# Kernel optimization log

Hardware: AMD Instinct MI355X
Metric: run time of the kernel (lower is better)

## Reference

```python
import jax, jax.numpy as jnp
import numpy as np

B, LQ, LKV, D, H = 4, 1024, 2048, 1024, 16
HD = D // H
EPS = 1e-5
NEG = -1e9


def _layernorm(x, w, b):
    mu = jnp.mean(x, axis=-1, keepdims=True)
    var = jnp.mean(jnp.square(x - mu), axis=-1, keepdims=True)
    return (x - mu) * jax.lax.rsqrt(var + EPS) * w + b


def setup_inputs() -> dict:
    key = jax.random.key(0)
    ks = jax.random.split(key, 10)
    q = jax.random.normal(ks[0], (B, LQ, D), dtype=jnp.float32)
    kv = jax.random.normal(ks[1], (B, LKV, D), dtype=jnp.float32)
    # ragged kv lengths; mask True == padding
    lengths = jax.random.randint(ks[2], (B,), LKV // 4, LKV + 1)
    mask = jnp.arange(LKV)[None, :] >= lengths[:, None]  # [B, LKV] bool
    s = 1.0 / np.sqrt(D)
    params = dict(
        norm_q_w=jnp.ones((D,), jnp.float32),
        norm_q_b=jnp.zeros((D,), jnp.float32),
        norm_kv_w=jnp.ones((D,), jnp.float32),
        norm_kv_b=jnp.zeros((D,), jnp.float32),
        Wq=jax.random.normal(ks[3], (D, D), jnp.float32) * s,
        bq=jnp.zeros((D,), jnp.float32),
        Wkv=jax.random.normal(ks[4], (2 * D, D), jnp.float32) * s,
        bkv=jnp.zeros((2 * D,), jnp.float32),
        Wo=jax.random.normal(ks[5], (D, D), jnp.float32) * s,
        bo=jnp.zeros((D,), jnp.float32),
    )
    return dict(q=q, kv=kv, mask=mask, **params)


def reference(q, kv, mask, norm_q_w, norm_q_b, norm_kv_w, norm_kv_b, Wq, bq, Wkv, bkv, Wo, bo):
    q_res = q
    qn = _layernorm(q, norm_q_w, norm_q_b)
    kvn = _layernorm(kv, norm_kv_w, norm_kv_b)
    # projections
    qh = (qn @ Wq.T + bq).reshape(B, LQ, H, HD)
    kvp = (kvn @ Wkv.T + bkv).reshape(B, LKV, 2, H, HD)
    k, v = kvp[:, :, 0], kvp[:, :, 1]  # [B, LKV, H, HD]
    # masked cross attention (math-equivalent to varlen flash attn over unpadded kv)
    scale = 1.0 / np.sqrt(HD)
    scores = jnp.einsum('bqhd,bkhd->bhqk', qh, k) * scale
    scores = jnp.where(mask[:, None, None, :], NEG, scores)
    attn = jax.nn.softmax(scores, axis=-1)
    out = jnp.einsum('bhqk,bkhd->bqhd', attn, v).reshape(B, LQ, D)
    # out proj + residual (dropout is identity in eval)
    return q_res + (out @ Wo.T + bo)


if __name__ == '__main__':
    inp = setup_inputs()
    y = reference(**inp)
    print(y.shape, y.dtype)
```

## Files before the change

kernel.cpp:

```cpp
#include <hip/hip_runtime.h>

#define DEV __device__ __forceinline__

typedef unsigned short u16;
typedef float  floatx4 __attribute__((ext_vector_type(4)));
typedef unsigned int uintx4 __attribute__((ext_vector_type(4)));
typedef __bf16 bf16x8 __attribute__((ext_vector_type(8)));

constexpr int cB = 4, cLQ = 1024, cLKV = 2048, cD = 1024, cH = 16, cHD = 64;

DEV u16 f2bf(float f) {
  unsigned u = __builtin_bit_cast(unsigned, f);
  u += 0x7fffu + ((u >> 16) & 1u);
  return (u16)(u >> 16);
}

DEV float bf2f(u16 u) {
  return __builtin_bit_cast(float, (unsigned)u << 16);
}

DEV bf16x8 ld_frag(const u16* p) {
  uintx4 u = *(const uintx4*)p;
  return __builtin_bit_cast(bf16x8, u);
}

DEV floatx4 mfma16(bf16x8 a, bf16x8 b, floatx4 c) {
  return __builtin_amdgcn_mfma_f32_16x16x32_bf16(a, b, c, 0, 0, 0);
}

__global__ __launch_bounds__(256) void ln_all_kernel(
    const float* __restrict__ q, const float* __restrict__ kv,
    const float* __restrict__ nqw, const float* __restrict__ nqb,
    const float* __restrict__ nkw, const float* __restrict__ nkb,
    u16* __restrict__ qn, u16* __restrict__ kvn) {
  int row = blockIdx.x, tid = threadIdx.x;
  const float* x; const float* w; const float* b; u16* dst;
  if (row < cB * cLQ) {
    x = q + (size_t)row * cD; w = nqw; b = nqb; dst = qn + (size_t)row * cD;
  } else {
    int r2 = row - cB * cLQ;
    x = kv + (size_t)r2 * cD; w = nkw; b = nkb; dst = kvn + (size_t)r2 * cD;
  }
  float4 v = ((const float4*)x)[tid];
  __shared__ float sbuf[8];
  float s = v.x + v.y + v.z + v.w;
  #pragma unroll
  for (int m = 1; m < 64; m <<= 1) s += __shfl_xor(s, m, 64);
  if ((tid & 63) == 0) sbuf[tid >> 6] = s;
  __syncthreads();
  float mean = (sbuf[0] + sbuf[1] + sbuf[2] + sbuf[3]) * (1.f / cD);
  float dx = v.x - mean, dy = v.y - mean, dz = v.z - mean, dw = v.w - mean;
  float ss = dx * dx + dy * dy + dz * dz + dw * dw;
  #pragma unroll
  for (int m = 1; m < 64; m <<= 1) ss += __shfl_xor(ss, m, 64);
  if ((tid & 63) == 0) sbuf[4 + (tid >> 6)] = ss;
  __syncthreads();
  float var = (sbuf[4] + sbuf[5] + sbuf[6] + sbuf[7]) * (1.f / cD);
  float rs = rsqrtf(var + 1e-5f);
  float4 wv = ((const float4*)w)[tid];
  float4 bv = ((const float4*)b)[tid];
  ushort4 o;
  o.x = f2bf(dx * rs * wv.x + bv.x);
  o.y = f2bf(dy * rs * wv.y + bv.y);
  o.z = f2bf(dz * rs * wv.z + bv.z);
  o.w = f2bf(dw * rs * wv.w + bv.w);
  ((ushort4*)dst)[tid] = o;
}

__global__ __launch_bounds__(256) void cast_lens_kernel(
    const float* __restrict__ Wq, const float* __restrict__ Wkv,
    const float* __restrict__ Wo, u16* __restrict__ wqb,
    u16* __restrict__ wkvb, u16* __restrict__ wob,
    const void* __restrict__ mask, int* __restrict__ lens) {
  int tid = threadIdx.x;
  if (blockIdx.x == 4096) {
    __shared__ int smode;
    __shared__ int cnt[cB];
    if (tid == 0) smode = 0;
    if (tid < cB) cnt[tid] = 0;
    __syncthreads();
    const unsigned* mi = (const unsigned*)mask;
    int bad = 0;
    for (int i = tid; i < cB * cLKV / 4; i += 256)
      if (mi[i] > 1u) bad = 1;
    if (bad) smode = 1;
    __syncthreads();
    if (smode == 0) {
      for (int b = 0; b < cB; b++) {
        int c = 0;
        for (int i = tid; i < cLKV; i += 256) c += (mi[(size_t)b * cLKV + i] == 0u);
        atomicAdd(&cnt[b], c);
      }
    } else {
      const unsigned char* m8 = (const unsigned char*)mask;
      for (int b = 0; b < cB; b++) {
        int c = 0;
        for (int i = tid; i < cLKV; i += 256) c += (m8[(size_t)b * cLKV + i] == 0);
        atomicAdd(&cnt[b], c);
      }
    }
    __syncthreads();
    if (tid < cB) lens[tid] = cnt[tid];
    return;
  }
  int gi = blockIdx.x * 256 + tid;
  const float* src; u16* dst; int off;
  if (gi < 262144)      { src = Wq;  dst = wqb;  off = gi; }
  else if (gi < 786432) { src = Wkv; dst = wkvb; off = gi - 262144; }
  else                  { src = Wo;  dst = wob;  off = gi - 786432; }
  float4 v = ((const float4*)src)[off];
  ushort4 o;
  o.x = f2bf(v.x); o.y = f2bf(v.y); o.z = f2bf(v.z); o.w = f2bf(v.w);
  ((ushort4*)dst)[off] = o;
}

struct TileCtx {
  int m16, quad, wr, wc;
};

DEV void gemm_mainloop(const u16* __restrict__ A, const u16* __restrict__ Bm,
                       int row0, int col0, int K, u16* As, u16* Bs,
                       const TileCtx& t, floatx4 (&acc)[4][4]) {
  int tid = threadIdx.x;
  int wave = tid >> 6, lane = tid & 63;
  int srow = wave * 16 + (lane >> 2);
  int sseg = (lane & 3) * 8;
  const u16* ga = A + (size_t)(row0 + srow) * K + sseg;
  const u16* gb = Bm + (size_t)(col0 + srow) * K + sseg;
  const size_t rstep = (size_t)64 * K;
  u16* wA = As + srow * 32 + sseg;
  u16* wB = Bs + srow * 32 + sseg;

  uintx4 a0 = *(const uintx4*)ga;
  uintx4 a1 = *(const uintx4*)(ga + rstep);
  uintx4 b0 = *(const uintx4*)gb;
  uintx4 b1 = *(const uintx4*)(gb + rstep);

  for (int k0 = 0; k0 < K; k0 += 32) {
    __syncthreads();
    *(uintx4*)wA = a0;
    *(uintx4*)(wA + 64 * 32) = a1;
    *(uintx4*)wB = b0;
    *(uintx4*)(wB + 64 * 32) = b1;
    if (k0 + 32 < K) {
      a0 = *(const uintx4*)(ga + k0 + 32);
      a1 = *(const uintx4*)(ga + rstep + k0 + 32);
      b0 = *(const uintx4*)(gb + k0 + 32);
      b1 = *(const uintx4*)(gb + rstep + k0 + 32);
    }
    __syncthreads();
    bf16x8 af[4], bfr[4];
    #pragma unroll
    for (int i = 0; i < 4; i++)
      af[i] = ld_frag(&As[(t.wr * 64 + i * 16 + t.m16) * 32 + t.quad * 8]);
    #pragma unroll
    for (int j = 0; j < 4; j++)
      bfr[j] = ld_frag(&Bs[(t.wc * 64 + j * 16 + t.m16) * 32 + t.quad * 8]);
    #pragma unroll
    for (int i = 0; i < 4; i++)
      #pragma unroll
      for (int j = 0; j < 4; j++)
        acc[i][j] = mfma16(af[i], bfr[j], acc[i][j]);
  }
}

__global__ __launch_bounds__(256) void proj_fused(
    const u16* __restrict__ qn, const u16* __restrict__ wqb,
    const float* __restrict__ bq, u16* __restrict__ qhb,
    const u16* __restrict__ kvn, const u16* __restrict__ wkvb,
    const float* __restrict__ bkv, u16* __restrict__ khb,
    u16* __restrict__ vthb) {
  __shared__ __align__(16) u16 As[128 * 32];
  __shared__ __align__(16) u16 Bs[128 * 32];
  int bid = blockIdx.x;
  int lane = threadIdx.x & 63;
  TileCtx t;
  t.m16 = lane & 15; t.quad = lane >> 4;
  int wave = threadIdx.x >> 6;
  t.wr = wave >> 1; t.wc = wave & 1;

  bool isQ = bid < 256;
  int row0, col0;
  const u16* A; const u16* Bm; const float* bias;
  if (isQ) {
    row0 = (bid >> 3) * 128; col0 = (bid & 7) * 128;
    A = qn; Bm = wqb; bias = bq;
  } else {
    int b2 = bid - 256;
    row0 = (b2 >> 4) * 128; col0 = (b2 & 15) * 128;
    A = kvn; Bm = wkvb; bias = bkv;
  }

  floatx4 z = {0.f, 0.f, 0.f, 0.f};
  floatx4 acc[4][4];
  #pragma unroll
  for (int i = 0; i < 4; i++)
    #pragma unroll
    for (int j = 0; j < 4; j++) acc[i][j] = z;

  gemm_mainloop(A, Bm, row0, col0, cD, As, Bs, t, acc);

  #pragma unroll
  for (int j = 0; j < 4; j++) {
    int col = col0 + t.wc * 64 + j * 16 + t.m16;
    float bs = bias[col];
    if (isQ) {
      #pragma unroll
      for (int i = 0; i < 4; i++) {
        int crow = row0 + t.wr * 64 + i * 16 + t.quad * 4;
        #pragma unroll
        for (int r = 0; r < 4; r++)
          qhb[(size_t)(crow + r) * cD + col] = f2bf((acc[i][j][r] + bs) * 0.125f);
      }
    } else {
      bool isK = col < cD;
      int c2 = isK ? col : col - cD;
      int hh = c2 >> 6, dd = c2 & 63;
      #pragma unroll
      for (int i = 0; i < 4; i++) {
        int crow = row0 + t.wr * 64 + i * 16 + t.quad * 4;
        int bb = crow >> 11, kvp = crow & (cLKV - 1);
        if (isK) {
          u16* dst = khb + ((size_t)(bb * cH + hh) * cLKV + kvp) * 64 + dd;
          #pragma unroll
          for (int r = 0; r < 4; r++) dst[(size_t)r * 64] = f2bf(acc[i][j][r] + bs);
        } else {
          u16* dst = vthb + ((size_t)(bb * cH + hh) * 64 + dd) * cLKV + kvp;
          ushort4 o;
          o.x = f2bf(acc[i][j][0] + bs);
          o.y = f2bf(acc[i][j][1] + bs);
          o.z = f2bf(acc[i][j][2] + bs);
          o.w = f2bf(acc[i][j][3] + bs);
          *(ushort4*)dst = o;
        }
      }
    }
  }
}

__global__ __launch_bounds__(256) void gemm_o(
    const u16* __restrict__ A, const u16* __restrict__ Bm,
    const float* __restrict__ bias, const float* __restrict__ res,
    float* __restrict__ Cout, int N, int K) {
  __shared__ __align__(16) u16 As[128 * 32];
  __shared__ __align__(16) u16 Bs[128 * 32];
  int lane = threadIdx.x & 63;
  TileCtx t;
  t.m16 = lane & 15; t.quad = lane >> 4;
  int wave = threadIdx.x >> 6;
  t.wr = wave >> 1; t.wc = wave & 1;
  int row0 = blockIdx.y * 128, col0 = blockIdx.x * 128;

  floatx4 z = {0.f, 0.f, 0.f, 0.f};
  floatx4 acc[4][4];
  #pragma unroll
  for (int i = 0; i < 4; i++)
    #pragma unroll
    for (int j = 0; j < 4; j++) acc[i][j] = z;

  gemm_mainloop(A, Bm, row0, col0, K, As, Bs, t, acc);

  #pragma unroll
  for (int j = 0; j < 4; j++) {
    int col = col0 + t.wc * 64 + j * 16 + t.m16;
    float bs = bias[col];
    #pragma unroll
    for (int i = 0; i < 4; i++) {
      int crow = row0 + t.wr * 64 + i * 16 + t.quad * 4;
      #pragma unroll
      for (int r = 0; r < 4; r++) {
        size_t idx = (size_t)(crow + r) * N + col;
        Cout[idx] = acc[i][j][r] + bs + res[idx];
      }
    }
  }
}

constexpr int KS = 72;

template<bool MASK>
DEV void attn_compute(int k0g, int len, const u16* __restrict__ Kt,
                      const u16* __restrict__ Vt, u16* __restrict__ psw,
                      bf16x8 aq0, bf16x8 aq1, int m16, int quad,
                      float (&lsum)[4], floatx4 (&accO)[4]) {
  floatx4 z = {0.f, 0.f, 0.f, 0.f};
  floatx4 s[4];
  #pragma unroll
  for (int t = 0; t < 4; t++) {
    bf16x8 bk0 = ld_frag(&Kt[(t * 16 + m16) * KS + quad * 8]);
    bf16x8 bk1 = ld_frag(&Kt[(t * 16 + m16) * KS + 32 + quad * 8]);
    floatx4 tt = z;
    tt = mfma16(aq0, bk0, tt);
    tt = mfma16(aq1, bk1, tt);
    s[t] = tt;
  }
  #pragma unroll
  for (int r = 0; r < 4; r++) {
    float e0, e1, e2, e3;
    if (MASK) {
      int key = k0g + m16;
      e0 = (key < len) ? __expf(s[0][r]) : 0.f;
      e1 = (key + 16 < len) ? __expf(s[1][r]) : 0.f;
      e2 = (key + 32 < len) ? __expf(s[2][r]) : 0.f;
      e3 = (key + 48 < len) ? __expf(s[3][r]) : 0.f;
    } else {
      e0 = __expf(s[0][r]);
      e1 = __expf(s[1][r]);
      e2 = __expf(s[2][r]);
      e3 = __expf(s[3][r]);
    }
    lsum[r] += (e0 + e1) + (e2 + e3);
    int prow = (quad * 4 + r) * KS + m16;
    psw[prow] = f2bf(e0);
    psw[prow + 16] = f2bf(e1);
    psw[prow + 32] = f2bf(e2);
    psw[prow + 48] = f2bf(e3);
  }
  bf16x8 ap0 = ld_frag(&psw[m16 * KS + quad * 8]);
  bf16x8 ap1 = ld_frag(&psw[m16 * KS + 32 + quad * 8]);
  #pragma unroll
  for (int db = 0; db < 4; db++) {
    bf16x8 bv0 = ld_frag(&Vt[(db * 16 + m16) * KS + quad * 8]);
    bf16x8 bv1 = ld_frag(&Vt[(db * 16 + m16) * KS + 32 + quad * 8]);
    accO[db] = mfma16(ap0, bv0, accO[db]);
    accO[db] = mfma16(ap1, bv1, accO[db]);
  }
}

__global__ __launch_bounds__(256) void attn_kernel(
    const u16* __restrict__ qh, const u16* __restrict__ kh,
    const u16* __restrict__ vth, const int* __restrict__ lens,
    u16* __restrict__ op, float* __restrict__ ls) {
  int gid = blockIdx.x;
  int b = gid & (cB - 1);
  int s = (gid >> 2) & 1;
  int h = (gid >> 3) & (cH - 1);
  int qt = gid >> 7;
  int len = lens[b];
  int koff = s << 10;
  int lim = min(len, koff + 1024);
  int nch = (lim > koff) ? ((lim - koff + 63) >> 6) : 0;

  int wave = threadIdx.x >> 6, lane = threadIdx.x & 63;
  int m16 = lane & 15, quad = lane >> 4;

  __shared__ __align__(16) u16 Kt[64 * KS];
  __shared__ __align__(16) u16 Vt[64 * KS];
  __shared__ __align__(16) u16 Ps[4][16 * KS];
  u16* psw = &Ps[wave][0];

  int qrow = qt * 64 + wave * 16 + m16;
  const u16* qp = qh + ((size_t)(b * cLQ + qrow) * cH + h) * cHD;
  bf16x8 aq0 = ld_frag(qp + quad * 8);
  bf16x8 aq1 = ld_frag(qp + 32 + quad * 8);

  const u16* kbase = kh + (size_t)(b * cH + h) * cLKV * cHD;
  const u16* vbase = vth + (size_t)(b * cH + h) * cHD * cLKV;

  int srow = threadIdx.x >> 3;
  int sseg = threadIdx.x & 7;
  const u16* kg0 = kbase + (size_t)srow * cHD + sseg * 8;
  const u16* vg0 = vbase + (size_t)srow * cLKV + sseg * 8;

  float lsum[4] = {0.f, 0.f, 0.f, 0.f};
  floatx4 z = {0.f, 0.f, 0.f, 0.f};
  floatx4 accO[4] = {z, z, z, z};

  uintx4 ka  = *(const uintx4*)(kg0 + (size_t)koff * cHD);
  uintx4 kb2 = *(const uintx4*)(kg0 + (size_t)(koff + 32) * cHD);
  uintx4 va  = *(const uintx4*)(vg0 + koff);
  uintx4 vb  = *(const uintx4*)(vg0 + (size_t)32 * cLKV + koff);

  for (int c = 0; c < nch; c++) {
    int k0g = koff + c * 64;
    __syncthreads();
    *(uintx4*)&Kt[srow * KS + sseg * 8] = ka;
    *(uintx4*)&Kt[(srow + 32) * KS + sseg * 8] = kb2;
    *(uintx4*)&Vt[srow * KS + sseg * 8] = va;
    *(uintx4*)&Vt[(srow + 32) * KS + sseg * 8] = vb;
    if (c + 1 < nch) {
      int kn = k0g + 64;
      ka  = *(const uintx4*)(kg0 + (size_t)kn * cHD);
      kb2 = *(const uintx4*)(kg0 + (size_t)(kn + 32) * cHD);
      va  = *(const uintx4*)(vg0 + kn);
      vb  = *(const uintx4*)(vg0 + (size_t)32 * cLKV + kn);
    }
    __syncthreads();
    if (k0g + 64 <= len)
      attn_compute<false>(k0g, len, Kt, Vt, psw, aq0, aq1, m16, quad, lsum, accO);
    else
      attn_compute<true>(k0g, len, Kt, Vt, psw, aq0, aq1, m16, quad, lsum, accO);
  }

  #pragma unroll
  for (int r = 0; r < 4; r++) {
    float t = lsum[r];
    #pragma unroll
    for (int m = 1; m < 16; m <<= 1) t += __shfl_xor(t, m, 64);
    lsum[r] = t;
  }

  #pragma unroll
  for (int r = 0; r < 4; r++) {
    int qg = qt * 64 + wave * 16 + quad * 4 + r;
    size_t rowidx = (size_t)(b * cLQ + qg);
    if (m16 == 0)
      ls[(size_t)s * cB * cLQ * cH + rowidx * cH + h] = lsum[r];
    size_t base = ((size_t)s * cB * cLQ + rowidx) * cD + h * 64;
    #pragma unroll
    for (int db = 0; db < 4; db++)
      op[base + db * 16 + m16] = f2bf(accO[db][r]);
  }
}

__global__ __launch_bounds__(256) void combine_kernel(
    const u16* __restrict__ op, const float* __restrict__ ls,
    u16* __restrict__ aob) {
  int row = blockIdx.x;
  int t = threadIdx.x;
  int h = t >> 4;
  float l = ls[(size_t)row * cH + h] + ls[(size_t)cB * cLQ * cH + (size_t)row * cH + h];
  float inv = 1.0f / l;
  size_t i0 = (size_t)row * cD + t * 4;
  ushort4 a = *(const ushort4*)(op + i0);
  ushort4 b2 = *(const ushort4*)(op + (size_t)cB * cLQ * cD + i0);
  ushort4 o;
  o.x = f2bf((bf2f(a.x) + bf2f(b2.x)) * inv);
  o.y = f2bf((bf2f(a.y) + bf2f(b2.y)) * inv);
  o.z = f2bf((bf2f(a.z) + bf2f(b2.z)) * inv);
  o.w = f2bf((bf2f(a.w) + bf2f(b2.w)) * inv);
  *(ushort4*)(aob + i0) = o;
}

extern "C" void kernel_launch(void* const* d_in, const int* in_sizes, int n_in,
                              void* d_out, int out_size, void* d_ws, size_t ws_size,
                              hipStream_t stream) {
  const float* q    = (const float*)d_in[0];
  const float* kv   = (const float*)d_in[1];
  const void*  mask = d_in[2];
  const float* nqw  = (const float*)d_in[3];
  const float* nqb  = (const float*)d_in[4];
  const float* nkw  = (const float*)d_in[5];
  const float* nkb  = (const float*)d_in[6];
  const float* Wq   = (const float*)d_in[7];
  const float* bq   = (const float*)d_in[8];
  const float* Wkv  = (const float*)d_in[9];
  const float* bkv  = (const float*)d_in[10];
  const float* Wo   = (const float*)d_in[11];
  const float* bo   = (const float*)d_in[12];
  float* out = (float*)d_out;

  char* w = (char*)d_ws;
  int* lens = (int*)w;       w += 256;
  u16* qn   = (u16*)w;       w += (size_t)cB * cLQ * cD * 2;
  u16* kvn  = (u16*)w;       w += (size_t)cB * cLKV * cD * 2;
  u16* wqb  = (u16*)w;       w += (size_t)cD * cD * 2;
  u16* wkvb = (u16*)w;       w += (size_t)2 * cD * cD * 2;
  u16* wob  = (u16*)w;       w += (size_t)cD * cD * 2;
  u16* qhb  = (u16*)w;       w += (size_t)cB * cLQ * cD * 2;
  u16* khb  = (u16*)w;       w += (size_t)cB * cH * cLKV * cHD * 2;
  u16* vthb = (u16*)w;       w += (size_t)cB * cH * cHD * cLKV * 2;
  u16* aob  = (u16*)w;       w += (size_t)cB * cLQ * cD * 2;
  u16* opart = (u16*)w;      w += (size_t)2 * cB * cLQ * cD * 2;
  float* lspart = (float*)w;

  ln_all_kernel<<<cB * (cLQ + cLKV), 256, 0, stream>>>(
      q, kv, nqw, nqb, nkw, nkb, qn, kvn);
  cast_lens_kernel<<<4097, 256, 0, stream>>>(
      Wq, Wkv, Wo, wqb, wkvb, wob, mask, lens);
  proj_fused<<<1280, 256, 0, stream>>>(
      qn, wqb, bq, qhb, kvn, wkvb, bkv, khb, vthb);
  attn_kernel<<<2048, 256, 0, stream>>>(
      qhb, khb, vthb, lens, opart, lspart);
  combine_kernel<<<cB * cLQ, 256, 0, stream>>>(opart, lspart, aob);
  gemm_o<<<dim3(cD / 128, cB * cLQ / 128), 256, 0, stream>>>(
      aob, wob, bo, q, out, cD, cD);
}
```

Measured before the change: 315.6 us.

## Merge prep kernels, double-buffer GEMM LDS, drop attention KV split and combine

```diff
diff --git a/kernel.cpp b/kernel.cpp
--- a/kernel.cpp
+++ b/kernel.cpp
@@ -15,8 +15,8 @@
   return (u16)(u >> 16);
 }
 
-DEV float bf2f(u16 u) {
-  return __builtin_bit_cast(float, (unsigned)u << 16);
+DEV u16 f2bf_t(float f) {
+  return (u16)(__builtin_bit_cast(unsigned, f) >> 16);
 }
 
 DEV bf16x8 ld_frag(const u16* p) {
@@ -28,52 +28,59 @@
   return __builtin_amdgcn_mfma_f32_16x16x32_bf16(a, b, c, 0, 0, 0);
 }
 
-__global__ __launch_bounds__(256) void ln_all_kernel(
+__global__ __launch_bounds__(256) void prep_kernel(
     const float* __restrict__ q, const float* __restrict__ kv,
     const float* __restrict__ nqw, const float* __restrict__ nqb,
     const float* __restrict__ nkw, const float* __restrict__ nkb,
-    u16* __restrict__ qn, u16* __restrict__ kvn) {
-  int row = blockIdx.x, tid = threadIdx.x;
-  const float* x; const float* w; const float* b; u16* dst;
-  if (row < cB * cLQ) {
-    x = q + (size_t)row * cD; w = nqw; b = nqb; dst = qn + (size_t)row * cD;
-  } else {
-    int r2 = row - cB * cLQ;
-    x = kv + (size_t)r2 * cD; w = nkw; b = nkb; dst = kvn + (size_t)r2 * cD;
-  }
-  float4 v = ((const float4*)x)[tid];
-  __shared__ float sbuf[8];
-  float s = v.x + v.y + v.z + v.w;
-  #pragma unroll
-  for (int m = 1; m < 64; m <<= 1) s += __shfl_xor(s, m, 64);
-  if ((tid & 63) == 0) sbuf[tid >> 6] = s;
-  __syncthreads();
-  float mean = (sbuf[0] + sbuf[1] + sbuf[2] + sbuf[3]) * (1.f / cD);
-  float dx = v.x - mean, dy = v.y - mean, dz = v.z - mean, dw = v.w - mean;
-  float ss = dx * dx + dy * dy + dz * dz + dw * dw;
-  #pragma unroll
-  for (int m = 1; m < 64; m <<= 1) ss += __shfl_xor(ss, m, 64);
-  if ((tid & 63) == 0) sbuf[4 + (tid >> 6)] = ss;
-  __syncthreads();
-  float var = (sbuf[4] + sbuf[5] + sbuf[6] + sbuf[7]) * (1.f / cD);
-  float rs = rsqrtf(var + 1e-5f);
-  float4 wv = ((const float4*)w)[tid];
-  float4 bv = ((const float4*)b)[tid];
-  ushort4 o;
-  o.x = f2bf(dx * rs * wv.x + bv.x);
-  o.y = f2bf(dy * rs * wv.y + bv.y);
-  o.z = f2bf(dz * rs * wv.z + bv.z);
-  o.w = f2bf(dw * rs * wv.w + bv.w);
-  ((ushort4*)dst)[tid] = o;
-}
-
-__global__ __launch_bounds__(256) void cast_lens_kernel(
+    u16* __restrict__ qn, u16* __restrict__ kvn,
     const float* __restrict__ Wq, const float* __restrict__ Wkv,
     const float* __restrict__ Wo, u16* __restrict__ wqb,
     u16* __restrict__ wkvb, u16* __restrict__ wob,
     const void* __restrict__ mask, int* __restrict__ lens) {
-  int tid = threadIdx.x;
-  if (blockIdx.x == 4096) {
+  int bid = blockIdx.x, tid = threadIdx.x;
+  if (bid < cB * (cLQ + cLKV)) {
+    const float* x; const float* w; const float* b; u16* dst;
+    if (bid < cB * cLQ) {
+      x = q + (size_t)bid * cD; w = nqw; b = nqb; dst = qn + (size_t)bid * cD;
+    } else {
+      int r2 = bid - cB * cLQ;
+      x = kv + (size_t)r2 * cD; w = nkw; b = nkb; dst = kvn + (size_t)r2 * cD;
+    }
+    float4 v = ((const float4*)x)[tid];
+    __shared__ float sbuf[8];
+    float s = v.x + v.y + v.z + v.w;
+    #pragma unroll
+    for (int m = 1; m < 64; m <<= 1) s += __shfl_xor(s, m, 64);
+    if ((tid & 63) == 0) sbuf[tid >> 6] = s;
+    __syncthreads();
+    float mean = (sbuf[0] + sbuf[1] + sbuf[2] + sbuf[3]) * (1.f / cD);
+    float dx = v.x - mean, dy = v.y - mean, dz = v.z - mean, dw = v.w - mean;
+    float ss = dx * dx + dy * dy + dz * dz + dw * dw;
+    #pragma unroll
+    for (int m = 1; m < 64; m <<= 1) ss += __shfl_xor(ss, m, 64);
+    if ((tid & 63) == 0) sbuf[4 + (tid >> 6)] = ss;
+    __syncthreads();
+    float var = (sbuf[4] + sbuf[5] + sbuf[6] + sbuf[7]) * (1.f / cD);
+    float rs = rsqrtf(var + 1e-5f);
+    float4 wv = ((const float4*)w)[tid];
+    float4 bv = ((const float4*)b)[tid];
+    ushort4 o;
+    o.x = f2bf(dx * rs * wv.x + bv.x);
+    o.y = f2bf(dy * rs * wv.y + bv.y);
+    o.z = f2bf(dz * rs * wv.z + bv.z);
+    o.w = f2bf(dw * rs * wv.w + bv.w);
+    ((ushort4*)dst)[tid] = o;
+  } else if (bid < cB * (cLQ + cLKV) + 4096) {
+    int gi = (bid - cB * (cLQ + cLKV)) * 256 + tid;
+    const float* src; u16* dst; int off;
+    if (gi < 262144)      { src = Wq;  dst = wqb;  off = gi; }
+    else if (gi < 786432) { src = Wkv; dst = wkvb; off = gi - 262144; }
+    else                  { src = Wo;  dst = wob;  off = gi - 786432; }
+    float4 v = ((const float4*)src)[off];
+    ushort4 o;
+    o.x = f2bf(v.x); o.y = f2bf(v.y); o.z = f2bf(v.z); o.w = f2bf(v.w);
+    ((ushort4*)dst)[off] = o;
+  } else {
     __shared__ int smode;
     __shared__ int cnt[cB];
     if (tid == 0) smode = 0;
@@ -101,17 +108,7 @@
     }
     __syncthreads();
     if (tid < cB) lens[tid] = cnt[tid];
-    return;
-  }
-  int gi = blockIdx.x * 256 + tid;
-  const float* src; u16* dst; int off;
-  if (gi < 262144)      { src = Wq;  dst = wqb;  off = gi; }
-  else if (gi < 786432) { src = Wkv; dst = wkvb; off = gi - 262144; }
-  else                  { src = Wo;  dst = wob;  off = gi - 786432; }
-  float4 v = ((const float4*)src)[off];
-  ushort4 o;
-  o.x = f2bf(v.x); o.y = f2bf(v.y); o.z = f2bf(v.z); o.w = f2bf(v.w);
-  ((ushort4*)dst)[off] = o;
+  }
 }
 
 struct TileCtx {
@@ -128,39 +125,53 @@
   const u16* ga = A + (size_t)(row0 + srow) * K + sseg;
   const u16* gb = Bm + (size_t)(col0 + srow) * K + sseg;
   const size_t rstep = (size_t)64 * K;
-  u16* wA = As + srow * 32 + sseg;
-  u16* wB = Bs + srow * 32 + sseg;
+  int woff = srow * 32 + sseg;
 
   uintx4 a0 = *(const uintx4*)ga;
   uintx4 a1 = *(const uintx4*)(ga + rstep);
   uintx4 b0 = *(const uintx4*)gb;
   uintx4 b1 = *(const uintx4*)(gb + rstep);
+  *(uintx4*)(As + woff) = a0;
+  *(uintx4*)(As + woff + 2048) = a1;
+  *(uintx4*)(Bs + woff) = b0;
+  *(uintx4*)(Bs + woff + 2048) = b1;
+  a0 = *(const uintx4*)(ga + 32);
+  a1 = *(const uintx4*)(ga + rstep + 32);
+  b0 = *(const uintx4*)(gb + 32);
+  b1 = *(const uintx4*)(gb + rstep + 32);
+  __syncthreads();
 
   for (int k0 = 0; k0 < K; k0 += 32) {
-    __syncthreads();
-    *(uintx4*)wA = a0;
-    *(uintx4*)(wA + 64 * 32) = a1;
-    *(uintx4*)wB = b0;
-    *(uintx4*)(wB + 64 * 32) = b1;
+    int cur = (k0 >> 5) & 1;
+    const u16* rA = As + cur * 4096;
+    const u16* rB = Bs + cur * 4096;
+    bf16x8 af[4], bfr[4];
+    #pragma unroll
+    for (int i = 0; i < 4; i++)
+      af[i] = ld_frag(&rA[(t.wr * 64 + i * 16 + t.m16) * 32 + t.quad * 8]);
+    #pragma unroll
+    for (int j = 0; j < 4; j++)
+      bfr[j] = ld_frag(&rB[(t.wc * 64 + j * 16 + t.m16) * 32 + t.quad * 8]);
     if (k0 + 32 < K) {
-      a0 = *(const uintx4*)(ga + k0 + 32);
-      a1 = *(const uintx4*)(ga + rstep + k0 + 32);
-      b0 = *(const uintx4*)(gb + k0 + 32);
-      b1 = *(const uintx4*)(gb + rstep + k0 + 32);
-    }
-    __syncthreads();
-    bf16x8 af[4], bfr[4];
-    #pragma unroll
-    for (int i = 0; i < 4; i++)
-      af[i] = ld_frag(&As[(t.wr * 64 + i * 16 + t.m16) * 32 + t.quad * 8]);
-    #pragma unroll
-    for (int j = 0; j < 4; j++)
-      bfr[j] = ld_frag(&Bs[(t.wc * 64 + j * 16 + t.m16) * 32 + t.quad * 8]);
+      u16* nA = As + (cur ^ 1) * 4096 + woff;
+      u16* nB = Bs + (cur ^ 1) * 4096 + woff;
+      *(uintx4*)nA = a0;
+      *(uintx4*)(nA + 2048) = a1;
+      *(uintx4*)nB = b0;
+      *(uintx4*)(nB + 2048) = b1;
+      if (k0 + 64 < K) {
+        a0 = *(const uintx4*)(ga + k0 + 64);
+        a1 = *(const uintx4*)(ga + rstep + k0 + 64);
+        b0 = *(const uintx4*)(gb + k0 + 64);
+        b1 = *(const uintx4*)(gb + rstep + k0 + 64);
+      }
+    }
     #pragma unroll
     for (int i = 0; i < 4; i++)
       #pragma unroll
       for (int j = 0; j < 4; j++)
         acc[i][j] = mfma16(af[i], bfr[j], acc[i][j]);
+    __syncthreads();
   }
 }
 
@@ -170,8 +181,8 @@
     const u16* __restrict__ kvn, const u16* __restrict__ wkvb,
     const float* __restrict__ bkv, u16* __restrict__ khb,
     u16* __restrict__ vthb) {
-  __shared__ __align__(16) u16 As[128 * 32];
-  __shared__ __align__(16) u16 Bs[128 * 32];
+  __shared__ __align__(16) u16 As[2 * 128 * 32];
+  __shared__ __align__(16) u16 Bs[2 * 128 * 32];
   int bid = blockIdx.x;
   int lane = threadIdx.x & 63;
   TileCtx t;
@@ -242,8 +253,8 @@
     const u16* __restrict__ A, const u16* __restrict__ Bm,
     const float* __restrict__ bias, const float* __restrict__ res,
     float* __restrict__ Cout, int N, int K) {
-  __shared__ __align__(16) u16 As[128 * 32];
-  __shared__ __align__(16) u16 Bs[128 * 32];
+  __shared__ __align__(16) u16 As[2 * 128 * 32];
+  __shared__ __align__(16) u16 Bs[2 * 128 * 32];
   int lane = threadIdx.x & 63;
   TileCtx t;
   t.m16 = lane & 15; t.quad = lane >> 4;
@@ -279,7 +290,7 @@
 constexpr int KS = 72;
 
 template<bool MASK>
-DEV void attn_compute(int k0g, int len, const u16* __restrict__ Kt,
+DEV void attn_compute(int k0, int len, const u16* __restrict__ Kt,
                       const u16* __restrict__ Vt, u16* __restrict__ psw,
                       bf16x8 aq0, bf16x8 aq1, int m16, int quad,
                       float (&lsum)[4], floatx4 (&accO)[4]) {
@@ -298,7 +309,7 @@
   for (int r = 0; r < 4; r++) {
     float e0, e1, e2, e3;
     if (MASK) {
-      int key = k0g + m16;
+      int key = k0 + m16;
       e0 = (key < len) ? __expf(s[0][r]) : 0.f;
       e1 = (key + 16 < len) ? __expf(s[1][r]) : 0.f;
       e2 = (key + 32 < len) ? __expf(s[2][r]) : 0.f;
@@ -311,10 +322,10 @@
     }
     lsum[r] += (e0 + e1) + (e2 + e3);
     int prow = (quad * 4 + r) * KS + m16;
-    psw[prow] = f2bf(e0);
-    psw[prow + 16] = f2bf(e1);
-    psw[prow + 32] = f2bf(e2);
-    psw[prow + 48] = f2bf(e3);
+    psw[prow] = f2bf_t(e0);
+    psw[prow + 16] = f2bf_t(e1);
+    psw[prow + 32] = f2bf_t(e2);
+    psw[prow + 48] = f2bf_t(e3);
   }
   bf16x8 ap0 = ld_frag(&psw[m16 * KS + quad * 8]);
   bf16x8 ap1 = ld_frag(&psw[m16 * KS + 32 + quad * 8]);
@@ -330,17 +341,12 @@
 __global__ __launch_bounds__(256) void attn_kernel(
     const u16* __restrict__ qh, const u16* __restrict__ kh,
     const u16* __restrict__ vth, const int* __restrict__ lens,
-    u16* __restrict__ op, float* __restrict__ ls) {
+    u16* __restrict__ out) {
   int gid = blockIdx.x;
   int b = gid & (cB - 1);
-  int s = (gid >> 2) & 1;
-  int h = (gid >> 3) & (cH - 1);
-  int qt = gid >> 7;
+  int h = (gid >> 2) & (cH - 1);
+  int qt = gid >> 6;
   int len = lens[b];
-  int koff = s << 10;
-  int lim = min(len, koff + 1024);
-  int nch = (lim > koff) ? ((lim - koff + 63) >> 6) : 0;
-
   int wave = threadIdx.x >> 6, lane = threadIdx.x & 63;
   int m16 = lane & 15, quad = lane >> 4;
 
@@ -359,37 +365,38 @@
 
   int srow = threadIdx.x >> 3;
   int sseg = threadIdx.x & 7;
-  const u16* kg0 = kbase + (size_t)srow * cHD + sseg * 8;
-  const u16* vg0 = vbase + (size_t)srow * cLKV + sseg * 8;
+  const u16* kg = kbase + (size_t)srow * cHD + sseg * 8;
+  const u16* vg = vbase + (size_t)srow * cLKV + sseg * 8;
 
   float lsum[4] = {0.f, 0.f, 0.f, 0.f};
   floatx4 z = {0.f, 0.f, 0.f, 0.f};
   floatx4 accO[4] = {z, z, z, z};
 
-  uintx4 ka  = *(const uintx4*)(kg0 + (size_t)koff * cHD);
-  uintx4 kb2 = *(const uintx4*)(kg0 + (size_t)(koff + 32) * cHD);
-  uintx4 va  = *(const uintx4*)(vg0 + koff);
-  uintx4 vb  = *(const uintx4*)(vg0 + (size_t)32 * cLKV + koff);
+  int nch = (len + 63) >> 6;
+  uintx4 ka  = *(const uintx4*)kg;
+  uintx4 kb2 = *(const uintx4*)(kg + (size_t)32 * cHD);
+  uintx4 va  = *(const uintx4*)vg;
+  uintx4 vb  = *(const uintx4*)(vg + (size_t)32 * cLKV);
 
   for (int c = 0; c < nch; c++) {
-    int k0g = koff + c * 64;
+    int k0 = c * 64;
     __syncthreads();
     *(uintx4*)&Kt[srow * KS + sseg * 8] = ka;
     *(uintx4*)&Kt[(srow + 32) * KS + sseg * 8] = kb2;
     *(uintx4*)&Vt[srow * KS + sseg * 8] = va;
     *(uintx4*)&Vt[(srow + 32) * KS + sseg * 8] = vb;
     if (c + 1 < nch) {
-      int kn = k0g + 64;
-      ka  = *(const uintx4*)(kg0 + (size_t)kn * cHD);
-      kb2 = *(const uintx4*)(kg0 + (size_t)(kn + 32) * cHD);
-      va  = *(const uintx4*)(vg0 + kn);
-      vb  = *(const uintx4*)(vg0 + (size_t)32 * cLKV + kn);
-    }
-    __syncthreads();
-    if (k0g + 64 <= len)
-      attn_compute<false>(k0g, len, Kt, Vt, psw, aq0, aq1, m16, quad, lsum, accO);
+      int kn = k0 + 64;
+      ka  = *(const uintx4*)(kg + (size_t)kn * cHD);
+      kb2 = *(const uintx4*)(kg + (size_t)(kn + 32) * cHD);
+      va  = *(const uintx4*)(vg + kn);
+      vb  = *(const uintx4*)(vg + (size_t)32 * cLKV + kn);
+    }
+    __syncthreads();
+    if (k0 + 64 <= len)
+      attn_compute<false>(k0, len, Kt, Vt, psw, aq0, aq1, m16, quad, lsum, accO);
     else
-      attn_compute<true>(k0g, len, Kt, Vt, psw, aq0, aq1, m16, quad, lsum, accO);
+      attn_compute<true>(k0, len, Kt, Vt, psw, aq0, aq1, m16, quad, lsum, accO);
   }
 
   #pragma unroll
@@ -402,34 +409,13 @@
 
   #pragma unroll
   for (int r = 0; r < 4; r++) {
+    float inv = 1.0f / lsum[r];
     int qg = qt * 64 + wave * 16 + quad * 4 + r;
-    size_t rowidx = (size_t)(b * cLQ + qg);
-    if (m16 == 0)
-      ls[(size_t)s * cB * cLQ * cH + rowidx * cH + h] = lsum[r];
-    size_t base = ((size_t)s * cB * cLQ + rowidx) * cD + h * 64;
+    size_t base = ((size_t)(b * cLQ + qg) * cH + h) * cHD;
     #pragma unroll
     for (int db = 0; db < 4; db++)
-      op[base + db * 16 + m16] = f2bf(accO[db][r]);
-  }
-}
-
-__global__ __launch_bounds__(256) void combine_kernel(
-    const u16* __restrict__ op, const float* __restrict__ ls,
-    u16* __restrict__ aob) {
-  int row = blockIdx.x;
-  int t = threadIdx.x;
-  int h = t >> 4;
-  float l = ls[(size_t)row * cH + h] + ls[(size_t)cB * cLQ * cH + (size_t)row * cH + h];
-  float inv = 1.0f / l;
-  size_t i0 = (size_t)row * cD + t * 4;
-  ushort4 a = *(const ushort4*)(op + i0);
-  ushort4 b2 = *(const ushort4*)(op + (size_t)cB * cLQ * cD + i0);
-  ushort4 o;
-  o.x = f2bf((bf2f(a.x) + bf2f(b2.x)) * inv);
-  o.y = f2bf((bf2f(a.y) + bf2f(b2.y)) * inv);
-  o.z = f2bf((bf2f(a.z) + bf2f(b2.z)) * inv);
-  o.w = f2bf((bf2f(a.w) + bf2f(b2.w)) * inv);
-  *(ushort4*)(aob + i0) = o;
+      out[base + db * 16 + m16] = f2bf(accO[db][r] * inv);
+  }
 }
 
 extern "C" void kernel_launch(void* const* d_in, const int* in_sizes, int n_in,
@@ -460,19 +446,15 @@
   u16* qhb  = (u16*)w;       w += (size_t)cB * cLQ * cD * 2;
   u16* khb  = (u16*)w;       w += (size_t)cB * cH * cLKV * cHD * 2;
   u16* vthb = (u16*)w;       w += (size_t)cB * cH * cHD * cLKV * 2;
-  u16* aob  = (u16*)w;       w += (size_t)cB * cLQ * cD * 2;
-  u16* opart = (u16*)w;      w += (size_t)2 * cB * cLQ * cD * 2;
-  float* lspart = (float*)w;
-
-  ln_all_kernel<<<cB * (cLQ + cLKV), 256, 0, stream>>>(
-      q, kv, nqw, nqb, nkw, nkb, qn, kvn);
-  cast_lens_kernel<<<4097, 256, 0, stream>>>(
+  u16* aob  = (u16*)w;
+
+  prep_kernel<<<cB * (cLQ + cLKV) + 4096 + 1, 256, 0, stream>>>(
+      q, kv, nqw, nqb, nkw, nkb, qn, kvn,
       Wq, Wkv, Wo, wqb, wkvb, wob, mask, lens);
   proj_fused<<<1280, 256, 0, stream>>>(
       qn, wqb, bq, qhb, kvn, wkvb, bkv, khb, vthb);
-  attn_kernel<<<2048, 256, 0, stream>>>(
-      qhb, khb, vthb, lens, opart, lspart);
-  combine_kernel<<<cB * cLQ, 256, 0, stream>>>(opart, lspart, aob);
+  attn_kernel<<<cB * cH * (cLQ / 64), 256, 0, stream>>>(
+      qhb, khb, vthb, lens, aob);
   gemm_o<<<dim3(cD / 128, cB * cLQ / 128), 256, 0, stream>>>(
       aob, wob, bo, q, out, cD, cD);
 }
```

Measured after the change: 278.2 us. -11.8%, faster.
